# Optimization experiments

Hardware: AMD Instinct MI355X
Metric: run time of the kernel (lower is better)

## Reference

```python
import jax, jax.numpy as jnp
import numpy as np

C = 128
H = 4
D = C // H
EPS = 1e-5


def setup_inputs() -> dict:
    key = jax.random.key(0)
    ks = jax.random.split(key, 9)
    B, S = 1, 256
    std = 1.0 / np.sqrt(C)
    return {
        "z_ij": jax.random.normal(ks[0], (B, S, S, C), dtype=jnp.float32),
        "ln_w": jnp.ones((C,), jnp.float32),
        "ln_b": jnp.zeros((C,), jnp.float32),
        "wq": jax.random.normal(ks[1], (C, C), jnp.float32) * std,
        "wk": jax.random.normal(ks[2], (C, C), jnp.float32) * std,
        "wv": jax.random.normal(ks[3], (C, C), jnp.float32) * std,
        "wb": jax.random.normal(ks[4], (C, H), jnp.float32) * std,
        "wg": jax.random.normal(ks[5], (C, C), jnp.float32) * std,
        "wo": jax.random.normal(ks[6], (C, C), jnp.float32) * std,
    }


def reference(z_ij, ln_w, ln_b, wq, wk, wv, wb, wg, wo):
    B, S = z_ij.shape[0], z_ij.shape[1]
    scale = 1.0 / np.sqrt(D)
    # LayerNorm over channel dim
    mu = jnp.mean(z_ij, axis=-1, keepdims=True)
    var = jnp.var(z_ij, axis=-1, keepdims=True)
    zn = (z_ij - mu) * jax.lax.rsqrt(var + EPS) * ln_w + ln_b
    # projections (weights stored input-major: x @ W)
    q = (zn @ wq).reshape(B, S, S, H, D)
    k = (zn @ wk).reshape(B, S, S, H, D)
    v = (zn @ wv).reshape(B, S, S, H, D)
    b = zn @ wb                      # (B,S,S,H)
    g = jax.nn.sigmoid(zn @ wg).reshape(B, S, S, H, D)
    # scores: q at (i,j) vs k at (j,k) -> (B,i,j,H,k); bias broadcast over k
    scores = jnp.einsum("bijhd,bjkhd->bijhk", q, k) * scale + b[..., None]
    alpha = jax.nn.softmax(scores, axis=-1)
    o = jnp.einsum("bijhk,bjkhd->bijhd", alpha, v)
    o = (g * o).reshape(B, S, S, C)
    return o @ wo
```

## Files before the change

kernel.cpp:

```cpp
#include <hip/hip_runtime.h>


#define NROWS 65536

typedef unsigned short u16;
typedef unsigned int   u32;
typedef __attribute__((ext_vector_type(8))) short short8;
typedef __attribute__((ext_vector_type(4))) float f32x4;
typedef __attribute__((ext_vector_type(4))) u32   u32x4;
typedef __attribute__((ext_vector_type(4))) u16   u16x4;
typedef __attribute__((ext_vector_type(8))) u16   u16x8;

__device__ __forceinline__ u16 f2bf(float x) {
    u32 u = __builtin_bit_cast(u32, x);
    return (u16)((u + 0x7fffu + ((u >> 16) & 1u)) >> 16);
}
__device__ __forceinline__ float bf2f(u16 h) {
    u32 u = (u32)h << 16;
    return __builtin_bit_cast(float, u);
}

__global__ __launch_bounds__(256) void prep_w(const float* __restrict__ wq,
                                              const float* __restrict__ wk,
                                              const float* __restrict__ wv,
                                              const float* __restrict__ wg,
                                              u16* __restrict__ wTh,
                                              u16* __restrict__ wTl)
{
    const int gid = blockIdx.x * 256 + threadIdx.x;
    const int k = gid >> 9, n = gid & 511;
    const float* Wm = (n < 128) ? wq : (n < 256) ? wk : (n < 384) ? wv : wg;
    float f = Wm[k * 128 + (n & 127)];
    if (n < 128) f *= 0.17677669529663687f;
    const u16 h = f2bf(f);
    wTh[n * 128 + k] = h;
    wTl[n * 128 + k] = f2bf(f - bf2f(h));
}

__global__ __launch_bounds__(1024) void lnproj_kernel(const float* __restrict__ z,
                                                      const float* __restrict__ lnw,
                                                      const float* __restrict__ lnb,
                                                      const u16* __restrict__ wTh,
                                                      const u16* __restrict__ wTl,
                                                      u16* __restrict__ qt2,
                                                      u16* __restrict__ kt2,
                                                      u16* __restrict__ vth,
                                                      u16* __restrict__ vtl,
                                                      float* __restrict__ gb)
{
    const int row0 = blockIdx.x * 128;
    const int tid  = threadIdx.x;

    __shared__ u16 Ah[16384];
    __shared__ u16 Al[16384];

    {
        const int c4 = (tid & 31) * 4;
        const float4 w4 = *(const float4*)(lnw + c4);
        const float4 b4 = *(const float4*)(lnb + c4);
        #pragma unroll
        for (int it = 0; it < 4; ++it) {
            const int row = it * 32 + (tid >> 5);
            const float4 v = *(const float4*)(z + (size_t)(row0 + row) * 128 + c4);
            float s  = v.x + v.y + v.z + v.w;
            float ss = v.x * v.x + v.y * v.y + v.z * v.z + v.w * v.w;
            #pragma unroll
            for (int off = 16; off > 0; off >>= 1) {
                s  += __shfl_xor(s,  off);
                ss += __shfl_xor(ss, off);
            }
            const float mu  = s * (1.0f / 128.0f);
            const float var = ss * (1.0f / 128.0f) - mu * mu;
            const float rs  = rsqrtf(var + 1e-5f);
            float o[4] = {(v.x - mu) * rs * w4.x + b4.x,
                          (v.y - mu) * rs * w4.y + b4.y,
                          (v.z - mu) * rs * w4.z + b4.z,
                          (v.w - mu) * rs * w4.w + b4.w};
            u16x4 hi, lo;
            #pragma unroll
            for (int c = 0; c < 4; ++c) {
                const u16 hx = f2bf(o[c]);
                hi[c] = hx;
                lo[c] = f2bf(o[c] - bf2f(hx));
            }
            const int slot = c4 >> 3, half = (c4 >> 2) & 1;
            const int phys = slot ^ (row & 15);
            *(u16x4*)&Ah[row * 128 + phys * 8 + half * 4] = hi;
            *(u16x4*)&Al[row * 128 + phys * 8 + half * 4] = lo;
        }
    }
    __syncthreads();

    const int w    = tid >> 6;
    const int wn   = w >> 1, wm = w & 1;
    const int lane = tid & 63;
    const int g    = lane >> 4;
    const int qc   = lane & 15;

    f32x4 acc[4][4];
    #pragma unroll
    for (int a = 0; a < 4; ++a)
        #pragma unroll
        for (int b = 0; b < 4; ++b) acc[a][b] = (f32x4){0.f, 0.f, 0.f, 0.f};

    #pragma unroll
    for (int kc = 0; kc < 4; ++kc) {
        short8 bh[4], bl[4];
        #pragma unroll
        for (int mt = 0; mt < 4; ++mt) {
            const int row  = wm * 64 + mt * 16 + qc;
            const int phys = (kc * 4 + g) ^ (row & 15);
            bh[mt] = *(const short8*)&Ah[row * 128 + phys * 8];
            bl[mt] = *(const short8*)&Al[row * 128 + phys * 8];
        }
        #pragma unroll
        for (int nt = 0; nt < 4; ++nt) {
            const int n_row = wn * 64 + nt * 16 + qc;
            const short8 ah = *(const short8*)(wTh + (size_t)n_row * 128 + kc * 32 + g * 8);
            const short8 al = *(const short8*)(wTl + (size_t)n_row * 128 + kc * 32 + g * 8);
            #pragma unroll
            for (int mt = 0; mt < 4; ++mt) {
                acc[nt][mt] = __builtin_amdgcn_mfma_f32_16x16x32_bf16(ah, bh[mt], acc[nt][mt], 0, 0, 0);
                acc[nt][mt] = __builtin_amdgcn_mfma_f32_16x16x32_bf16(ah, bl[mt], acc[nt][mt], 0, 0, 0);
                acc[nt][mt] = __builtin_amdgcn_mfma_f32_16x16x32_bf16(al, bh[mt], acc[nt][mt], 0, 0, 0);
            }
        }
    }

    #pragma unroll
    for (int nt = 0; nt < 4; ++nt) {
        const int nb  = wn * 64 + nt * 16 + g * 4;
        const int mat = nb >> 7;
        const int nn  = nb & 127;
        #pragma unroll
        for (int mt = 0; mt < 4; ++mt) {
            const int m = row0 + wm * 64 + mt * 16 + qc;
            const f32x4 a = acc[nt][mt];
            if (mat == 3) {
                float4 sg;
                sg.x = 1.0f / (1.0f + __expf(-a[0]));
                sg.y = 1.0f / (1.0f + __expf(-a[1]));
                sg.z = 1.0f / (1.0f + __expf(-a[2]));
                sg.w = 1.0f / (1.0f + __expf(-a[3]));
                *(float4*)(gb + (size_t)m * 128 + nn) = sg;
            } else {
                const int h = nn >> 5, d0 = nn & 31;
                if (mat == 2) {
                    const int j = m >> 8, kk = m & 255;
                    #pragma unroll
                    for (int r = 0; r < 4; ++r) {
                        const u16 hx = f2bf(a[r]);
                        const size_t idx = ((size_t)(j * 4 + h) * 32 + d0 + r) * 256 + kk;
                        vth[idx] = hx;
                        vtl[idx] = f2bf(a[r] - bf2f(hx));
                    }
                } else {
                    u16x4 hi, lo;
                    #pragma unroll
                    for (int c = 0; c < 4; ++c) {
                        const u16 hx = f2bf(a[c]);
                        hi[c] = hx;
                        lo[c] = f2bf(a[c] - bf2f(hx));
                    }
                    u16* dst;
                    if (mat == 0) {
                        const int i = m >> 8, j = m & 255;
                        dst = qt2 + ((size_t)(j * 4 + h) * 256 + i) * 64 + d0;
                    } else {
                        const int j = m >> 8, kk = m & 255;
                        dst = kt2 + ((size_t)(j * 4 + h) * 256 + kk) * 64 + d0;
                    }
                    *(u16x4*)dst        = hi;
                    *(u16x4*)(dst + 32) = lo;
                }
            }
        }
    }
}

__global__ __launch_bounds__(1024) void attn_kernel(const u16* __restrict__ qt2,
                                                    const u16* __restrict__ kt2,
                                                    const u16* __restrict__ vth,
                                                    const u16* __restrict__ vtl,
                                                    const float* __restrict__ gb,
                                                    float* __restrict__ go)
{
    const int jh   = blockIdx.x;
    const int tid  = threadIdx.x;
    const int q0   = (tid >> 6) * 16;
    const int lane = tid & 63;
    const int g    = lane >> 4;
    const int qc   = lane & 15;

    __shared__ u16 Ks[16384];
    __shared__ u16 Vs[16384];

    {
        const u16* kg = kt2 + (size_t)jh * 16384;
        #pragma unroll
        for (int it = 0; it < 2; ++it) {
            const int t   = it * 1024 + tid;
            const int row = t >> 3, c = t & 7;
            const int dc  = c ^ (row & 7);
            *(u16x8*)&Ks[row * 64 + dc * 8] = *(const u16x8*)(kg + t * 8);
        }
        const u16* vhg = vth + (size_t)jh * 8192;
        const u16* vlg = vtl + (size_t)jh * 8192;
        {
            const int t   = tid;
            const int row = t >> 5, c = t & 31;
            const int dc  = (c & 24) | ((c & 7) ^ (row & 7));
            *(u16x8*)&Vs[row * 256 + dc * 8] = *(const u16x8*)(vhg + t * 8);
        }
        {
            const int t   = tid;
            const int row = t >> 5, c = t & 31;
            const int dc  = (c & 24) | ((c & 7) ^ (row & 7));
            *(u16x8*)&Vs[8192 + row * 256 + dc * 8] = *(const u16x8*)(vlg + t * 8);
        }
    }

    const u16* qrow = qt2 + ((size_t)jh * 256 + q0 + qc) * 64;
    const short8 bqh = *(const short8*)(qrow + g * 8);
    const short8 bql = *(const short8*)(qrow + 32 + g * 8);

    __syncthreads();

    f32x4 st[16];
    #pragma unroll
    for (int t = 0; t < 16; ++t) st[t] = (f32x4){0.f, 0.f, 0.f, 0.f};

    const int slotH = (g ^ (qc & 7)) * 8;
    #pragma unroll
    for (int kt = 0; kt < 16; ++kt) {
        const int rbase = (kt * 16 + qc) * 64;
        const short8 ah = *(const short8*)&Ks[rbase + slotH];
        const short8 al = *(const short8*)&Ks[rbase + (slotH ^ 32)];
        st[kt] = __builtin_amdgcn_mfma_f32_16x16x32_bf16(ah, bqh, st[kt], 0, 0, 0);
        st[kt] = __builtin_amdgcn_mfma_f32_16x16x32_bf16(ah, bql, st[kt], 0, 0, 0);
        st[kt] = __builtin_amdgcn_mfma_f32_16x16x32_bf16(al, bqh, st[kt], 0, 0, 0);
    }

    float m = -1e30f;
    #pragma unroll
    for (int t = 0; t < 16; ++t)
        #pragma unroll
        for (int r = 0; r < 4; ++r) m = fmaxf(m, st[t][r]);
    m = fmaxf(m, __shfl_xor(m, 16));
    m = fmaxf(m, __shfl_xor(m, 32));

    float l = 0.0f;
    #pragma unroll
    for (int t = 0; t < 16; ++t)
        #pragma unroll
        for (int r = 0; r < 4; ++r) {
            const float p = __expf(st[t][r] - m);
            st[t][r] = p;
            l += p;
        }
    l += __shfl_xor(l, 16);
    l += __shfl_xor(l, 32);
    const float inv = 1.0f / l;
    #pragma unroll
    for (int t = 0; t < 16; ++t)
        #pragma unroll
        for (int r = 0; r < 4; ++r) st[t][r] *= inv;

    f32x4 o0 = (f32x4){0.f, 0.f, 0.f, 0.f};
    f32x4 o1 = (f32x4){0.f, 0.f, 0.f, 0.f};
    const int  slA   = qc + 16 * (2 * (g & 1));
    const int  slB   = slA + 16;
    const bool upper = (g >> 1) != 0;

    #pragma unroll
    for (int kc = 0; kc < 8; ++kc) {
        u32 pkh[2][2];
        #pragma unroll
        for (int tt = 0; tt < 2; ++tt)
            #pragma unroll
            for (int u = 0; u < 2; ++u) {
                const float x = st[2 * kc + tt][2 * u];
                const float y = st[2 * kc + tt][2 * u + 1];
                pkh[tt][u] = (u32)f2bf(x) | ((u32)f2bf(y) << 16);
            }
        u32x4 AH;
        #pragma unroll
        for (int j = 0; j < 4; ++j) {
            const int u  = j & 1;
            const int sl = (j < 2) ? slA : slB;
            const u32 h0 = (u32)__shfl((int)pkh[0][u], sl);
            const u32 h1 = (u32)__shfl((int)pkh[1][u], sl);
            AH[j] = upper ? h1 : h0;
        }
        const short8 pah = __builtin_bit_cast(short8, AH);

        const int vc    = (((kc & 1) * 4 + g) ^ (qc & 7));
        const int vslot = ((kc >> 1) * 8 + vc) * 8;
        const short8 b0h = *(const short8*)&Vs[        qc * 256 + vslot];
        const short8 b0l = *(const short8*)&Vs[8192 +  qc * 256 + vslot];
        const short8 b1h = *(const short8*)&Vs[       (16 + qc) * 256 + vslot];
        const short8 b1l = *(const short8*)&Vs[8192 + (16 + qc) * 256 + vslot];
        o0 = __builtin_amdgcn_mfma_f32_16x16x32_bf16(pah, b0h, o0, 0, 0, 0);
        o0 = __builtin_amdgcn_mfma_f32_16x16x32_bf16(pah, b0l, o0, 0, 0, 0);
        o1 = __builtin_amdgcn_mfma_f32_16x16x32_bf16(pah, b1h, o1, 0, 0, 0);
        o1 = __builtin_amdgcn_mfma_f32_16x16x32_bf16(pah, b1l, o1, 0, 0, 0);
    }

    const int jj = jh >> 2, h = jh & 3;
    #pragma unroll
    for (int r = 0; r < 4; ++r) {
        const int qg = q0 + g * 4 + r;
        const size_t base = ((size_t)qg * 256 + jj) * 128 + h * 32 + qc;
        go[base]      = gb[base]      * o0[r];
        go[base + 16] = gb[base + 16] * o1[r];
    }
}

__global__ __launch_bounds__(256) void out_kernel(const float* __restrict__ A,
                                                  const float* __restrict__ W,
                                                  float* __restrict__ out)
{
    const int by   = blockIdx.x;
    const int row0 = by * 128;

    __shared__ float As[32][132];
    __shared__ float Bs[32][132];

    const int tid = threadIdx.x;
    const int tm  = tid & 15, tn = tid >> 4;
    const int m0  = tm * 4,  n0 = tn * 4;

    float acc[8][8];
    #pragma unroll
    for (int a = 0; a < 8; ++a)
        #pragma unroll
        for (int q = 0; q < 8; ++q) acc[a][q] = 0.0f;

    for (int kc = 0; kc < 128; kc += 32) {
        __syncthreads();
        #pragma unroll
        for (int it = 0; it < 4; ++it) {
            const int id = it * 256 + tid;
            const int m  = id >> 3;
            const int kq = (id & 7) * 4;
            const float4 a4 = *(const float4*)(A + (size_t)(row0 + m) * 128 + kc + kq);
            As[kq + 0][m] = a4.x; As[kq + 1][m] = a4.y;
            As[kq + 2][m] = a4.z; As[kq + 3][m] = a4.w;
        }
        #pragma unroll
        for (int it = 0; it < 4; ++it) {
            const int id = it * 256 + tid;
            const int kk = id >> 5;
            const int c4 = (id & 31) * 4;
            *(float4*)&Bs[kk][c4] = *(const float4*)(W + (size_t)(kc + kk) * 128 + c4);
        }
        __syncthreads();
        #pragma unroll
        for (int k = 0; k < 32; ++k) {
            const float4 a0 = *(const float4*)&As[k][m0];
            const float4 a1 = *(const float4*)&As[k][m0 + 64];
            const float4 b0 = *(const float4*)&Bs[k][n0];
            const float4 b1 = *(const float4*)&Bs[k][n0 + 64];
            const float av[8] = {a0.x, a0.y, a0.z, a0.w, a1.x, a1.y, a1.z, a1.w};
            const float bv[8] = {b0.x, b0.y, b0.z, b0.w, b1.x, b1.y, b1.z, b1.w};
            #pragma unroll
            for (int ii = 0; ii < 8; ++ii)
                #pragma unroll
                for (int jj = 0; jj < 8; ++jj)
                    acc[ii][jj] += av[ii] * bv[jj];
        }
    }

    #pragma unroll
    for (int ii = 0; ii < 8; ++ii) {
        const int mA = (ii < 4) ? (m0 + ii) : (m0 + 60 + ii);
        const int r  = row0 + mA;
        #pragma unroll
        for (int nh = 0; nh < 2; ++nh) {
            const int c0 = n0 + nh * 64;
            float4 vv;
            vv.x = acc[ii][nh * 4 + 0]; vv.y = acc[ii][nh * 4 + 1];
            vv.z = acc[ii][nh * 4 + 2]; vv.w = acc[ii][nh * 4 + 3];
            *(float4*)(out + (size_t)r * 128 + c0) = vv;
        }
    }
}

extern "C" void kernel_launch(void* const* d_in, const int* in_sizes, int n_in,
                              void* d_out, int out_size, void* d_ws, size_t ws_size,
                              hipStream_t stream)
{
    const float* z   = (const float*)d_in[0];
    const float* lnw = (const float*)d_in[1];
    const float* lnb = (const float*)d_in[2];
    const float* wq  = (const float*)d_in[3];
    const float* wk  = (const float*)d_in[4];
    const float* wv  = (const float*)d_in[5];
    const float* wg  = (const float*)d_in[7];
    const float* wo  = (const float*)d_in[8];

    const size_t T = (size_t)NROWS * 128;
    float* go  = (float*)d_ws;
    u16*   wTh = (u16*)d_ws;
    u16*   wTl = wTh + 512 * 128;
    float* gb  = (float*)d_ws + T;
    u16*   qt2 = (u16*)(gb + T);
    u16*   kt2 = qt2 + 2 * T;
    u16*   vth = kt2 + 2 * T;
    u16*   vtl = vth + T;

    prep_w       <<<256,          256, 0, stream>>>(wq, wk, wv, wg, wTh, wTl);
    lnproj_kernel<<<512,         1024, 0, stream>>>(z, lnw, lnb, wTh, wTl,
                                                    qt2, kt2, vth, vtl, gb);
    attn_kernel  <<<1024,        1024, 0, stream>>>(qt2, kt2, vth, vtl, gb, go);
    out_kernel   <<<512,          256, 0, stream>>>(go, wo, (float*)d_out);
}
```

Before: 159.1 us.

## Stage projection epilogue through shared memory for coalesced Q/K/V/gate stores

The epilogue of the LN+projection kernel no longer writes Q, K, V hi/lo and the gate directly from MFMA accumulators with scattered 8-byte or 2-byte stores. Each matrix is staged in turn through a swizzled shared-memory buffer, then written out with 16-byte vector stores that are contiguous in the transposed output layouts. This targets uncoalesced global writes, especially the per-element V transpose. The cost is several extra __syncthreads and LDS round-trips, plus the assumption that each block's 128 rows fall inside a single i row.

```diff
diff --git a/kernel.cpp b/kernel.cpp
--- a/kernel.cpp
+++ b/kernel.cpp
@@ -51,8 +51,9 @@
     const int row0 = blockIdx.x * 128;
     const int tid  = threadIdx.x;
 
-    __shared__ u16 Ah[16384];
-    __shared__ u16 Al[16384];
+    __shared__ __align__(16) u16 S[32768];
+    u16* Ah = S;
+    u16* Al = S + 16384;
 
     {
         const int c4 = (tid & 31) * 4;
@@ -126,54 +127,146 @@
             }
         }
     }
-
-    #pragma unroll
-    for (int nt = 0; nt < 4; ++nt) {
-        const int nb  = wn * 64 + nt * 16 + g * 4;
-        const int mat = nb >> 7;
-        const int nn  = nb & 127;
-        #pragma unroll
-        for (int mt = 0; mt < 4; ++mt) {
-            const int m = row0 + wm * 64 + mt * 16 + qc;
-            const f32x4 a = acc[nt][mt];
-            if (mat == 3) {
-                float4 sg;
-                sg.x = 1.0f / (1.0f + __expf(-a[0]));
-                sg.y = 1.0f / (1.0f + __expf(-a[1]));
-                sg.z = 1.0f / (1.0f + __expf(-a[2]));
-                sg.w = 1.0f / (1.0f + __expf(-a[3]));
-                *(float4*)(gb + (size_t)m * 128 + nn) = sg;
-            } else {
-                const int h = nn >> 5, d0 = nn & 31;
-                if (mat == 2) {
-                    const int j = m >> 8, kk = m & 255;
+    __syncthreads();
+
+    const int matw = w >> 2;
+    const int wl   = wn & 1;
+    const int iblk = blockIdx.x >> 1;
+    const int base = (blockIdx.x & 1) * 128;
+
+    if (matw == 0) {
+        #pragma unroll
+        for (int nt = 0; nt < 4; ++nt) {
+            const int np = wl * 64 + nt * 16 + g * 4;
+            const int h  = np >> 5, d0 = np & 31;
+            const int sh = d0 >> 3, ins = d0 & 7;
+            #pragma unroll
+            for (int mt = 0; mt < 4; ++mt) {
+                const int ml  = wm * 64 + mt * 16 + qc;
+                const int row = ml * 4 + h;
+                const int key = (row ^ (row >> 2)) & 7;
+                const f32x4 a = acc[nt][mt];
+                u16x4 hi, lo;
+                #pragma unroll
+                for (int c = 0; c < 4; ++c) {
+                    const u16 hx = f2bf(a[c]);
+                    hi[c] = hx;
+                    lo[c] = f2bf(a[c] - bf2f(hx));
+                }
+                *(u16x4*)&S[row * 64 + ((sh    ) ^ key) * 8 + ins] = hi;
+                *(u16x4*)&S[row * 64 + ((sh + 4) ^ key) * 8 + ins] = lo;
+            }
+        }
+    }
+    __syncthreads();
+    #pragma unroll
+    for (int it = 0; it < 4; ++it) {
+        const int idx = it * 1024 + tid;
+        const int row = idx >> 3, slot = idx & 7;
+        const int key = (row ^ (row >> 2)) & 7;
+        const u16x8 d = *(const u16x8*)&S[row * 64 + (slot ^ key) * 8];
+        const int ml = row >> 2, h = row & 3;
+        *(u16x8*)(qt2 + ((size_t)((base + ml) * 4 + h) * 256 + iblk) * 64 + slot * 8) = d;
+    }
+    __syncthreads();
+
+    if (matw == 1) {
+        #pragma unroll
+        for (int nt = 0; nt < 4; ++nt) {
+            const int np = wl * 64 + nt * 16 + g * 4;
+            const int h  = np >> 5, d0 = np & 31;
+            const int sh = d0 >> 3, ins = d0 & 7;
+            #pragma unroll
+            for (int mt = 0; mt < 4; ++mt) {
+                const int ml  = wm * 64 + mt * 16 + qc;
+                const int row = h * 128 + ml;
+                const int key = (row ^ (row >> 2)) & 7;
+                const f32x4 a = acc[nt][mt];
+                u16x4 hi, lo;
+                #pragma unroll
+                for (int c = 0; c < 4; ++c) {
+                    const u16 hx = f2bf(a[c]);
+                    hi[c] = hx;
+                    lo[c] = f2bf(a[c] - bf2f(hx));
+                }
+                *(u16x4*)&S[row * 64 + ((sh    ) ^ key) * 8 + ins] = hi;
+                *(u16x4*)&S[row * 64 + ((sh + 4) ^ key) * 8 + ins] = lo;
+            }
+        }
+    }
+    __syncthreads();
+    #pragma unroll
+    for (int it = 0; it < 4; ++it) {
+        const int idx = it * 1024 + tid;
+        const int row = idx >> 3, slot = idx & 7;
+        const int key = (row ^ (row >> 2)) & 7;
+        const u16x8 d = *(const u16x8*)&S[row * 64 + (slot ^ key) * 8];
+        const int h = row >> 7, kk = row & 127;
+        *(u16x8*)(kt2 + ((size_t)(iblk * 4 + h) * 256 + base + kk) * 64 + slot * 8) = d;
+    }
+    __syncthreads();
+
+    #pragma unroll
+    for (int sel = 0; sel < 2; ++sel) {
+        if (matw == 2) {
+            #pragma unroll
+            for (int nt = 0; nt < 4; ++nt) {
+                const int np = wl * 64 + nt * 16 + g * 4;
+                const int h  = np >> 5, d0 = np & 31;
+                #pragma unroll
+                for (int mt = 0; mt < 4; ++mt) {
+                    const int ml = wm * 64 + mt * 16 + qc;
+                    const f32x4 a = acc[nt][mt];
                     #pragma unroll
                     for (int r = 0; r < 4; ++r) {
                         const u16 hx = f2bf(a[r]);
-                        const size_t idx = ((size_t)(j * 4 + h) * 32 + d0 + r) * 256 + kk;
-                        vth[idx] = hx;
-                        vtl[idx] = f2bf(a[r] - bf2f(hx));
+                        const u16 vv = sel ? f2bf(a[r] - bf2f(hx)) : hx;
+                        S[(h * 32 + d0 + r) * 136 + ml] = vv;
                     }
-                } else {
-                    u16x4 hi, lo;
-                    #pragma unroll
-                    for (int c = 0; c < 4; ++c) {
-                        const u16 hx = f2bf(a[c]);
-                        hi[c] = hx;
-                        lo[c] = f2bf(a[c] - bf2f(hx));
-                    }
-                    u16* dst;
-                    if (mat == 0) {
-                        const int i = m >> 8, j = m & 255;
-                        dst = qt2 + ((size_t)(j * 4 + h) * 256 + i) * 64 + d0;
-                    } else {
-                        const int j = m >> 8, kk = m & 255;
-                        dst = kt2 + ((size_t)(j * 4 + h) * 256 + kk) * 64 + d0;
-                    }
-                    *(u16x4*)dst        = hi;
-                    *(u16x4*)(dst + 32) = lo;
                 }
             }
+        }
+        __syncthreads();
+        u16* dstm = sel ? vtl : vth;
+        #pragma unroll
+        for (int it = 0; it < 2; ++it) {
+            const int idx = it * 1024 + tid;
+            const int row = idx >> 4, chunk = idx & 15;
+            const u16x8 d = *(const u16x8*)&S[row * 136 + chunk * 8];
+            const int h = row >> 5, dd = row & 31;
+            *(u16x8*)(dstm + ((size_t)(iblk * 4 + h) * 32 + dd) * 256 + base + chunk * 8) = d;
+        }
+        __syncthreads();
+    }
+
+    {
+        float* F = (float*)S;
+        if (matw == 3) {
+            #pragma unroll
+            for (int nt = 0; nt < 4; ++nt) {
+                const int np = wl * 64 + nt * 16 + g * 4;
+                #pragma unroll
+                for (int mt = 0; mt < 4; ++mt) {
+                    const int ml  = wm * 64 + mt * 16 + qc;
+                    const int key = (ml ^ (ml >> 2)) & 7;
+                    const f32x4 a = acc[nt][mt];
+                    float4 sg;
+                    sg.x = 1.0f / (1.0f + __expf(-a[0]));
+                    sg.y = 1.0f / (1.0f + __expf(-a[1]));
+                    sg.z = 1.0f / (1.0f + __expf(-a[2]));
+                    sg.w = 1.0f / (1.0f + __expf(-a[3]));
+                    *(float4*)&F[ml * 128 + (((np >> 2) ^ key)) * 4] = sg;
+                }
+            }
+        }
+        __syncthreads();
+        #pragma unroll
+        for (int it = 0; it < 4; ++it) {
+            const int idx = it * 1024 + tid;
+            const int row = idx >> 5, slot = idx & 31;
+            const int key = (row ^ (row >> 2)) & 7;
+            const float4 d = *(const float4*)&F[row * 128 + (slot ^ key) * 4];
+            *(float4*)(gb + (size_t)(row0 + row) * 128 + slot * 4) = d;
         }
     }
 }
```

Result: slower. 163.1 us (+2.5%).
